# Optimization experiments

Measured on AMD Instinct MI355X. Metric: run time of the kernel, lower is better.

Reference implementation:

```python
import jax, jax.numpy as jnp
import numpy as np

N_ATOMS = 4096
HSIZE = 128
N_HEADS = 8
D_K = HSIZE // N_HEADS


def setup_inputs() -> dict:
    key = jax.random.key(0)
    ks = jax.random.split(key, 11)
    s = 1.0 / np.sqrt(HSIZE)
    return {
        "query": jax.random.normal(ks[0], (N_ATOMS, HSIZE), dtype=jnp.float32),
        "key": jax.random.normal(ks[1], (N_ATOMS, HSIZE), dtype=jnp.float32),
        "value": jax.random.normal(ks[2], (N_ATOMS, HSIZE), dtype=jnp.float32),
        "mask": jax.random.randint(ks[3], (N_ATOMS, N_ATOMS), 0, 2, dtype=jnp.int32),
        "Wq": jax.random.normal(ks[4], (HSIZE, HSIZE), dtype=jnp.float32) * s,
        "bq": jnp.zeros((HSIZE,), dtype=jnp.float32),
        "Wk": jax.random.normal(ks[5], (HSIZE, HSIZE), dtype=jnp.float32) * s,
        "bk": jnp.zeros((HSIZE,), dtype=jnp.float32),
        "Wv": jax.random.normal(ks[6], (HSIZE, HSIZE), dtype=jnp.float32) * s,
        "bv": jnp.zeros((HSIZE,), dtype=jnp.float32),
        "Wo": jax.random.normal(ks[7], (HSIZE, HSIZE), dtype=jnp.float32) * s,
    }


def _mha(query, key, value, mask, Wq, bq, Wk, bk, Wv, bv, Wo):
    n = query.shape[0]
    # project and split heads: [n, hsize] -> [H, n, d_k]
    def heads(x, W, b):
        return (x @ W.T + b).reshape(n, N_HEADS, D_K).transpose(1, 0, 2)
    q = heads(query, Wq, bq)
    k = heads(key, Wk, bk)
    v = heads(value, Wv, bv)
    scale = 1.0 / jnp.sqrt(jnp.asarray(D_K, q.dtype))
    scores = jnp.einsum("hnd,hmd->hnm", q, k) * scale  # [H, n, n]
    scores = jnp.where(mask[None, :, :] == 0, jnp.asarray(-1e9, scores.dtype), scores)
    p_attn = jax.nn.softmax(scores, axis=-1)
    x = jnp.einsum("hnm,hmd->hnd", p_attn, v)  # [H, n, d_k]
    x = x.transpose(1, 0, 2).reshape(n, HSIZE)  # merge heads
    return x @ Wo.T  # output_linear has bias=False


def reference(query, key, value, mask, Wq, bq, Wk, bk, Wv, bv, Wo):
    return _mha(query, key, value, mask, Wq, bq, Wk, bk, Wv, bv, Wo)
```

## Files before the change

### kernel.cpp

```cpp
#include <hip/hip_runtime.h>
#include <hip/hip_bf16.h>

#define NA 4096
#define HS 128
#define CSTR 136

typedef unsigned short u16;
typedef unsigned long long u64;
using bf16x8  = __attribute__((ext_vector_type(8))) short;
using f32x4   = __attribute__((ext_vector_type(4))) float;
using ushort8 = __attribute__((ext_vector_type(8))) unsigned short;
using u32x4   = __attribute__((ext_vector_type(4))) unsigned;

#define QSCALE 0.18033688011112042f

static __device__ __forceinline__ u16 f2bf(float f) {
    unsigned u = __builtin_bit_cast(unsigned, f);
    u += 0x7FFFu + ((u >> 16) & 1u);
    return (u16)(u >> 16);
}

static __device__ __forceinline__ unsigned pkbf(float a, float b) {
    float2 f; f.x = a; f.y = b;
    __hip_bfloat162 r = __float22bfloat162_rn(f);
    unsigned u;
    __builtin_memcpy(&u, &r, 4);
    return u;
}

__global__ __launch_bounds__(256) void proj_pack(
    const float* __restrict__ Xq, const float* __restrict__ Xk, const float* __restrict__ Xv,
    const float* __restrict__ Wq, const float* __restrict__ Wk,
    const float* __restrict__ Wv, const float* __restrict__ Wo,
    const float* __restrict__ bq, const float* __restrict__ bk,
    const float* __restrict__ bv, const int* __restrict__ mask,
    u16* __restrict__ Qbh, u16* __restrict__ Kbh, u16* __restrict__ VtB,
    u64* __restrict__ Mp, u16* __restrict__ WoF)
{
    const int blk = blockIdx.x;
    const int t = threadIdx.x;

    __shared__ __align__(16) u16 Ws[16384];
    __shared__ __align__(16) u16 Xs[32 * CSTR];
    __shared__ __align__(16) u16 Cs[32 * CSTR];

    if (blk < 1024) {
        const int wv = t >> 6, lane = t & 63;
        const int row = blk * 4 + wv;
        const int* mrow = mask + (size_t)row * NA;

        int4 v[16];
#pragma unroll
        for (int ch = 0; ch < 16; ++ch)
            v[ch] = *(const int4*)(mrow + ch * 256 + lane * 4);

        unsigned char* nibL = (unsigned char*)Xs + wv * 1024;
#pragma unroll
        for (int ch = 0; ch < 16; ++ch) {
            const unsigned nib = (v[ch].x != 0 ? 1u : 0u) | (v[ch].y != 0 ? 2u : 0u)
                               | (v[ch].z != 0 ? 4u : 0u) | (v[ch].w != 0 ? 8u : 0u);
            nibL[ch * 64 + lane] = (unsigned char)nib;
        }

        const uint4 b16 = *(const uint4*)(nibL + lane * 16);
        unsigned z[4];
        {
            const unsigned xs4[4] = { b16.x, b16.y, b16.z, b16.w };
#pragma unroll
            for (int i = 0; i < 4; ++i) {
                unsigned x = xs4[i];
                x = (x | (x >> 4)) & 0x00FF00FFu;
                x = (x | (x >> 8)) & 0x0000FFFFu;
                z[i] = x;
            }
        }
        const u64 word = (u64)(z[0] | (z[1] << 16))
                       | ((u64)(z[2] | (z[3] << 16)) << 32);
        Mp[(size_t)row * 64 + lane] = word;
        return;
    }

    if (blk >= 1408) {
        const int gid = (blk - 1408) * 256 + t;
        const int off = gid * 4;
        float4 v = *(const float4*)(Wo + off);
        ushort4 o;
        o.x = f2bf(v.x); o.y = f2bf(v.y); o.z = f2bf(v.z); o.w = f2bf(v.w);
        const int j = off >> 7, k0 = off & 127;
        const int j0 = j >> 4, c = j & 15, kk = k0 >> 5, q = (k0 >> 3) & 3;
        *(ushort4*)(WoF + ((j0 * 4 + kk) * 16 + c) * 32 + q * 8 + (k0 & 7)) = o;
        return;
    }

    const int pb = blk - 1024;
    const int mat = pb >> 7;
    const float* X = (mat == 0) ? Xq : (mat == 1) ? Xk : Xv;
    const float* Wsrc = (mat == 0) ? Wq : (mat == 1) ? Wk : Wv;
    const float* bsrc = (mat == 0) ? bq : (mat == 1) ? bk : bv;
    const float sc = (mat == 0) ? QSCALE : 1.0f;
    const int r0b = (pb & 127) * 32;

    {
        const int base = t * 64;
#pragma unroll
        for (int i = 0; i < 16; ++i) {
            const int off = base + i * 4;
            float4 v = *(const float4*)(Wsrc + off);
            ushort4 o;
            o.x = f2bf(v.x * sc); o.y = f2bf(v.y * sc);
            o.z = f2bf(v.z * sc); o.w = f2bf(v.w * sc);
            const int j = off >> 7, k0 = off & 127;
            const int j0 = j >> 4, c2 = j & 15, kk = k0 >> 5, qq = (k0 >> 3) & 3;
            *(ushort4*)(Ws + (j0 * 4 + kk) * 512 + qq * 128 + c2 * 8 + (k0 & 7)) = o;
        }
    }

    {
        const int r = t >> 3, cb = (t & 7) * 16;
        const float* Xr = X + (size_t)(r0b + r) * HS + cb;
#pragma unroll
        for (int seg = 0; seg < 4; ++seg) {
            float4 f = *(const float4*)(Xr + seg * 4);
            ushort4 u;
            u.x = f2bf(f.x); u.y = f2bf(f.y); u.z = f2bf(f.z); u.w = f2bf(f.w);
            *(ushort4*)(Xs + r * CSTR + cb + seg * 4) = u;
        }
    }
    __syncthreads();

    const int wv = t >> 6, lane = t & 63;
    const int c = lane & 15, q = lane >> 4;
    const int rw = (wv & 1) * 16;
    const int j0b = (wv >> 1) * 4;

    bf16x8 af[4];
#pragma unroll
    for (int kk = 0; kk < 4; ++kk)
        af[kk] = *(const bf16x8*)(Xs + (rw + c) * CSTR + kk * 32 + q * 8);

    const f32x4 zero = {0.f, 0.f, 0.f, 0.f};
#pragma unroll
    for (int jj = 0; jj < 4; ++jj) {
        const int j0 = j0b + jj;
        f32x4 acc = zero;
#pragma unroll
        for (int kk = 0; kk < 4; ++kk) {
            bf16x8 bf = *(const bf16x8*)(Ws + (j0 * 4 + kk) * 512 + q * 128 + c * 8);
            acc = __builtin_amdgcn_mfma_f32_16x16x32_bf16(af[kk], bf, acc, 0, 0, 0);
        }
        const float bias = bsrc[j0 * 16 + c] * sc;
#pragma unroll
        for (int r = 0; r < 4; ++r)
            Cs[(rw + 4 * q + r) * CSTR + j0 * 16 + c] = f2bf(acc[r] + bias);
    }
    __syncthreads();

    if (mat < 2) {
        u16* dst = (mat == 0) ? Qbh : Kbh;
        const int h8 = t >> 5, r = t & 31;
        const u16* src = Cs + r * CSTR + h8 * 16;
        int drow = r0b + r;
        if (mat == 1) {
            const int k = (r0b & 32) + r;
            const int slot = ((k >> 5) * 2 + ((k >> 2) & 1)) * 16
                           + ((k >> 3) & 3) * 4 + (k & 3);
            drow = (r0b & ~63) + slot;
        }
        u16* dp = dst + (size_t)h8 * (NA * 16) + (size_t)drow * 16;
        *(bf16x8*)(dp)     = *(const bf16x8*)(src);
        *(bf16x8*)(dp + 8) = *(const bf16x8*)(src + 8);
    } else {
        const int d = t >> 1, s = t & 1;
        const int kb = r0b >> 6, ko = (r0b & 32) + s * 16;
        ushort8 v0, v1;
#pragma unroll
        for (int jj = 0; jj < 8; ++jj) v0[jj] = Cs[(s * 16 + jj) * CSTR + d];
#pragma unroll
        for (int jj = 0; jj < 8; ++jj) v1[jj] = Cs[(s * 16 + 8 + jj) * CSTR + d];
        u16* dp = VtB + (size_t)kb * 8192 + d * 64 + ko;
        *(ushort8*)(dp)     = v0;
        *(ushort8*)(dp + 8) = v1;
    }
}

__global__ __launch_bounds__(256, 4) void attn(
    const u64* __restrict__ Mp,
    const u16* __restrict__ Qbh, const u16* __restrict__ Kbh, const u16* __restrict__ VtB,
    float* __restrict__ part)
{
    __shared__ __align__(8)  u64 Mwp[16 * 17];
    __shared__ __align__(8)  u64 Mtab[16];

    const int t = threadIdx.x;
    const int h = blockIdx.z * 4 + (t >> 6);
    const int lane = t & 63;
    const int c = lane & 15;
    const int q = lane >> 4;
    const int tile = blockIdx.x, split = blockIdx.y;
    const int i0 = tile * 16;
    const int kt0 = split * 1024;

    {
        const int row = t >> 4, w = t & 15;
        Mwp[row * 17 + w] = Mp[(size_t)(i0 + row) * 64 + (kt0 >> 6) + w];
    }
    if (t < 16) {
        const unsigned lo = ((t & 1) ? 0xFFFFu : 0u) | ((t & 2) ? 0xFFFF0000u : 0u);
        const unsigned hi = ((t & 4) ? 0xFFFFu : 0u) | ((t & 8) ? 0xFFFF0000u : 0u);
        Mtab[t] = (u64)lo | ((u64)hi << 32);
    }

    const u16* Qh = Qbh + (size_t)h * (NA * 16);
    const u16* Kh = Kbh + (size_t)h * (NA * 16);

    const bf16x8 qf = *(const bf16x8*)(Qh + (size_t)(i0 + c) * 16 + (q & 1) * 8);

    bf16x8 ones;
#pragma unroll
    for (int i = 0; i < 8; ++i) ones[i] = (short)0x3F80;

    __syncthreads();

    const f32x4 zero = {0.f, 0.f, 0.f, 0.f};
    f32x4 Oacc = zero;
    f32x4 Lacc = zero;

    bf16x8 kf[4];
#pragma unroll
    for (int t4 = 0; t4 < 4; ++t4)
        kf[t4] = *(const bf16x8*)(Kh + (size_t)(kt0 + t4 * 16 + c) * 16 + (q & 1) * 8);

#pragma unroll 1
    for (int it = 0; it < 16; ++it) {
        const int kt = kt0 + it * 64;
        const u16* Vb = VtB + (size_t)(kt >> 6) * 8192 + (h * 16 + c) * 64;

        bf16x8 vf0 = *(const bf16x8*)(Vb + q * 8);
        bf16x8 vf1 = *(const bf16x8*)(Vb + 32 + q * 8);

        f32x4 ST[4];
        __builtin_amdgcn_s_setprio(1);
#pragma unroll
        for (int t4 = 0; t4 < 4; ++t4)
            ST[t4] = __builtin_amdgcn_mfma_f32_16x16x32_bf16(kf[t4], qf, zero, 0, 0, 0);
        __builtin_amdgcn_s_setprio(0);

        const int ktn = kt0 + ((it + 1) & 15) * 64;
#pragma unroll
        for (int t4 = 0; t4 < 4; ++t4)
            kf[t4] = *(const bf16x8*)(Kh + (size_t)(ktn + t4 * 16 + c) * 16 + (q & 1) * 8);

        const u64 w = Mwp[c * 17 + it];
        const unsigned wa = (unsigned)(w >> (8 * q));
        const unsigned wb = (unsigned)(w >> (32 + 8 * q));

        unsigned pl[4], ph[4];
#pragma unroll
        for (int t4 = 0; t4 < 4; ++t4) {
            const unsigned nib = (((t4 & 2) ? wb : wa) >> ((t4 & 1) * 4)) & 15u;
            float p0 = __builtin_amdgcn_exp2f(ST[t4][0]);
            float p1 = __builtin_amdgcn_exp2f(ST[t4][1]);
            float p2 = __builtin_amdgcn_exp2f(ST[t4][2]);
            float p3 = __builtin_amdgcn_exp2f(ST[t4][3]);
            const unsigned lo = pkbf(p0, p1);
            const unsigned hi = pkbf(p2, p3);
            const u64 mex = Mtab[nib];
            pl[t4] = lo & (unsigned)mex;
            ph[t4] = hi & (unsigned)(mex >> 32);
        }
        const u32x4 a0 = { pl[0], ph[0], pl[1], ph[1] };
        const u32x4 a1 = { pl[2], ph[2], pl[3], ph[3] };
        const bf16x8 pf0 = __builtin_bit_cast(bf16x8, a0);
        const bf16x8 pf1 = __builtin_bit_cast(bf16x8, a1);

        __builtin_amdgcn_s_setprio(1);
        Oacc = __builtin_amdgcn_mfma_f32_16x16x32_bf16(pf0, vf0, Oacc, 0, 0, 0);
        Oacc = __builtin_amdgcn_mfma_f32_16x16x32_bf16(pf1, vf1, Oacc, 0, 0, 0);
        Lacc = __builtin_amdgcn_mfma_f32_16x16x32_bf16(pf0, ones, Lacc, 0, 0, 0);
        Lacc = __builtin_amdgcn_mfma_f32_16x16x32_bf16(pf1, ones, Lacc, 0, 0, 0);
        __builtin_amdgcn_s_setprio(0);
    }

    float* base = part + (size_t)((tile * 4 + split) * 8 + h) * 272;
#pragma unroll
    for (int r = 0; r < 4; ++r)
        base[(4 * q + r) * 16 + c] = Oacc[r];
    if (c == 0) {
#pragma unroll
        for (int r = 0; r < 4; ++r)
            base[256 + 4 * q + r] = Lacc[r];
    }
}

__global__ __launch_bounds__(256) void reduce_out(
    const float* __restrict__ part, const u16* __restrict__ WoF,
    float* __restrict__ out)
{
    __shared__ __align__(16) u16 xs[16 * CSTR];

    const int t = threadIdx.x;
    const int tile = blockIdx.x;
    const int i0 = tile * 16;
    const float* Pt = part + (size_t)tile * 4 * 8 * 272;

    {
        const int i = t >> 4, d = t & 15;
#pragma unroll
        for (int h = 0; h < 8; ++h) {
            float os = 0.f, ls = 0.f;
#pragma unroll
            for (int s = 0; s < 4; ++s) {
                const float* b = Pt + (size_t)(s * 8 + h) * 272;
                os += b[i * 16 + d];
                ls += b[256 + i];
            }
            xs[i * CSTR + h * 16 + d] = f2bf(os / ls);
        }
    }
    __syncthreads();

    const int wv = t >> 6, lane = t & 63;
    const int c = lane & 15, q = lane >> 4;

    bf16x8 af[4];
#pragma unroll
    for (int kk = 0; kk < 4; ++kk)
        af[kk] = *(const bf16x8*)(xs + c * CSTR + kk * 32 + q * 8);

    const f32x4 zero = {0.f, 0.f, 0.f, 0.f};
#pragma unroll
    for (int jj = 0; jj < 2; ++jj) {
        const int j0 = wv * 2 + jj;
        f32x4 acc = zero;
#pragma unroll
        for (int kk = 0; kk < 4; ++kk) {
            bf16x8 bf = *(const bf16x8*)(WoF + (j0 * 4 + kk) * 512 + c * 32 + q * 8);
            acc = __builtin_amdgcn_mfma_f32_16x16x32_bf16(af[kk], bf, acc, 0, 0, 0);
        }
#pragma unroll
        for (int r = 0; r < 4; ++r)
            out[(size_t)(i0 + 4 * q + r) * HS + j0 * 16 + c] = acc[r];
    }
}

extern "C" void kernel_launch(void* const* d_in, const int* in_sizes, int n_in,
                              void* d_out, int out_size, void* d_ws, size_t ws_size,
                              hipStream_t stream) {
    const float* query = (const float*)d_in[0];
    const float* key   = (const float*)d_in[1];
    const float* value = (const float*)d_in[2];
    const int*   mask  = (const int*)d_in[3];
    const float* Wq    = (const float*)d_in[4];
    const float* bq    = (const float*)d_in[5];
    const float* Wk    = (const float*)d_in[6];
    const float* bk    = (const float*)d_in[7];
    const float* Wv    = (const float*)d_in[8];
    const float* bv    = (const float*)d_in[9];
    const float* Wo    = (const float*)d_in[10];

    u16* Qbh = (u16*)d_ws;
    u16* Kbh = Qbh + (size_t)NA * HS;
    u16* VtB = Kbh + (size_t)NA * HS;
    u16* WoF = VtB + (size_t)NA * HS;
    u64*  Mp  = (u64*)(WoF + 16384);
    float* partb = (float*)(Mp + (size_t)NA * 64);

    proj_pack<<<1424, 256, 0, stream>>>(query, key, value, Wq, Wk, Wv, Wo,
                                        bq, bk, bv, mask,
                                        Qbh, Kbh, VtB, Mp, WoF);
    attn<<<dim3(256, 4, 2), 256, 0, stream>>>(Mp, Qbh, Kbh, VtB, partb);
    reduce_out<<<256, 256, 0, stream>>>(partb, WoF, (float*)d_out);
}
```

Baseline: 170.1 us.

## Fuse mask bit-packing into attention kernel and process all heads per block

```diff
diff --git a/kernel.cpp b/kernel.cpp
--- a/kernel.cpp
+++ b/kernel.cpp
@@ -33,9 +33,9 @@
     const float* __restrict__ Wq, const float* __restrict__ Wk,
     const float* __restrict__ Wv, const float* __restrict__ Wo,
     const float* __restrict__ bq, const float* __restrict__ bk,
-    const float* __restrict__ bv, const int* __restrict__ mask,
+    const float* __restrict__ bv,
     u16* __restrict__ Qbh, u16* __restrict__ Kbh, u16* __restrict__ VtB,
-    u64* __restrict__ Mp, u16* __restrict__ WoF)
+    u16* __restrict__ WoF)
 {
     const int blk = blockIdx.x;
     const int t = threadIdx.x;
@@ -44,44 +44,8 @@
     __shared__ __align__(16) u16 Xs[32 * CSTR];
     __shared__ __align__(16) u16 Cs[32 * CSTR];
 
-    if (blk < 1024) {
-        const int wv = t >> 6, lane = t & 63;
-        const int row = blk * 4 + wv;
-        const int* mrow = mask + (size_t)row * NA;
-
-        int4 v[16];
-#pragma unroll
-        for (int ch = 0; ch < 16; ++ch)
-            v[ch] = *(const int4*)(mrow + ch * 256 + lane * 4);
-
-        unsigned char* nibL = (unsigned char*)Xs + wv * 1024;
-#pragma unroll
-        for (int ch = 0; ch < 16; ++ch) {
-            const unsigned nib = (v[ch].x != 0 ? 1u : 0u) | (v[ch].y != 0 ? 2u : 0u)
-                               | (v[ch].z != 0 ? 4u : 0u) | (v[ch].w != 0 ? 8u : 0u);
-            nibL[ch * 64 + lane] = (unsigned char)nib;
-        }
-
-        const uint4 b16 = *(const uint4*)(nibL + lane * 16);
-        unsigned z[4];
-        {
-            const unsigned xs4[4] = { b16.x, b16.y, b16.z, b16.w };
-#pragma unroll
-            for (int i = 0; i < 4; ++i) {
-                unsigned x = xs4[i];
-                x = (x | (x >> 4)) & 0x00FF00FFu;
-                x = (x | (x >> 8)) & 0x0000FFFFu;
-                z[i] = x;
-            }
-        }
-        const u64 word = (u64)(z[0] | (z[1] << 16))
-                       | ((u64)(z[2] | (z[3] << 16)) << 32);
-        Mp[(size_t)row * 64 + lane] = word;
-        return;
-    }
-
-    if (blk >= 1408) {
-        const int gid = (blk - 1408) * 256 + t;
+    if (blk >= 384) {
+        const int gid = (blk - 384) * 256 + t;
         const int off = gid * 4;
         float4 v = *(const float4*)(Wo + off);
         ushort4 o;
@@ -92,7 +56,7 @@
         return;
     }
 
-    const int pb = blk - 1024;
+    const int pb = blk;
     const int mat = pb >> 7;
     const float* X = (mat == 0) ? Xq : (mat == 1) ? Xk : Xv;
     const float* Wsrc = (mat == 0) ? Wq : (mat == 1) ? Wk : Wv;
@@ -183,16 +147,17 @@
     }
 }
 
-__global__ __launch_bounds__(256, 4) void attn(
-    const u64* __restrict__ Mp,
+__global__ __launch_bounds__(512, 4) void attn(
+    const int* __restrict__ mask,
     const u16* __restrict__ Qbh, const u16* __restrict__ Kbh, const u16* __restrict__ VtB,
     float* __restrict__ part)
 {
     __shared__ __align__(8)  u64 Mwp[16 * 17];
     __shared__ __align__(8)  u64 Mtab[16];
+    __shared__ __align__(16) unsigned char Msc[8 * 512];
 
     const int t = threadIdx.x;
-    const int h = blockIdx.z * 4 + (t >> 6);
+    const int h = t >> 6;
     const int lane = t & 63;
     const int c = lane & 15;
     const int q = lane >> 4;
@@ -201,8 +166,35 @@
     const int kt0 = split * 1024;
 
     {
-        const int row = t >> 4, w = t & 15;
-        Mwp[row * 17 + w] = Mp[(size_t)(i0 + row) * 64 + (kt0 >> 6) + w];
+#pragma unroll
+        for (int rr = 0; rr < 2; ++rr) {
+            const int row = h * 2 + rr;
+            const int* mrow = mask + (size_t)(i0 + row) * NA + kt0;
+            unsigned char* dst = Msc + h * 512 + rr * 256;
+#pragma unroll
+            for (int ch = 0; ch < 4; ++ch) {
+                const int4 v = *(const int4*)(mrow + ch * 256 + lane * 4);
+                const unsigned nib = (v.x != 0 ? 1u : 0u) | (v.y != 0 ? 2u : 0u)
+                                   | (v.z != 0 ? 4u : 0u) | (v.w != 0 ? 8u : 0u);
+                dst[ch * 64 + lane] = (unsigned char)nib;
+            }
+        }
+        if (lane < 32) {
+            const int rr = lane >> 4, k = lane & 15;
+            const int row = h * 2 + rr;
+            const uint4 b16 = *(const uint4*)(Msc + h * 512 + rr * 256 + k * 16);
+            unsigned z[4];
+            const unsigned xs4[4] = { b16.x, b16.y, b16.z, b16.w };
+#pragma unroll
+            for (int i = 0; i < 4; ++i) {
+                unsigned x = xs4[i];
+                x = (x | (x >> 4)) & 0x00FF00FFu;
+                x = (x | (x >> 8)) & 0x0000FFFFu;
+                z[i] = x;
+            }
+            Mwp[row * 17 + k] = (u64)(z[0] | (z[1] << 16))
+                              | ((u64)(z[2] | (z[3] << 16)) << 32);
+        }
     }
     if (t < 16) {
         const unsigned lo = ((t & 1) ? 0xFFFFu : 0u) | ((t & 2) ? 0xFFFF0000u : 0u);
@@ -362,12 +354,10 @@
     u16* Kbh = Qbh + (size_t)NA * HS;
     u16* VtB = Kbh + (size_t)NA * HS;
     u16* WoF = VtB + (size_t)NA * HS;
-    u64*  Mp  = (u64*)(WoF + 16384);
-    float* partb = (float*)(Mp + (size_t)NA * 64);
-
-    proj_pack<<<1424, 256, 0, stream>>>(query, key, value, Wq, Wk, Wv, Wo,
-                                        bq, bk, bv, mask,
-                                        Qbh, Kbh, VtB, Mp, WoF);
-    attn<<<dim3(256, 4, 2), 256, 0, stream>>>(Mp, Qbh, Kbh, VtB, partb);
+    float* partb = (float*)(WoF + 16384);
+
+    proj_pack<<<400, 256, 0, stream>>>(query, key, value, Wq, Wk, Wv, Wo,
+                                       bq, bk, bv, Qbh, Kbh, VtB, WoF);
+    attn<<<dim3(256, 4), 512, 0, stream>>>(mask, Qbh, Kbh, VtB, partb);
     reduce_out<<<256, 256, 0, stream>>>(partb, WoF, (float*)d_out);
 }
```

New measurement: 168.1 us, median of 2. Within noise of the previous version (-1.2%).
